# Kernel optimization log

Hardware: AMD Instinct MI355X
Metric: run time of the kernel (lower is better)

## Reference

```python
import jax, jax.numpy as jnp
import numpy as np

N_NODES, F_IN, HID = 50000, 128, 64
N_EDGES = 400000


def _mean_agg(x, ei, n):
    # mean of src features over incoming edges per dst node
    src, dst = ei[0], ei[1]
    s = jax.ops.segment_sum(x[src], dst, num_segments=n)
    cnt = jax.ops.segment_sum(jnp.ones((ei.shape[1],), x.dtype), dst, num_segments=n)
    return s / jnp.maximum(cnt, 1.0)[:, None]


def _conv(x, ei, Wd, Ws, Wu):
    # HeteroGNNConv: mean-aggregate, then lin_dst(x_dst) || lin_src(aggr) -> lin_update
    agg = _mean_agg(x, ei, x.shape[0])
    comb = jnp.concatenate([x @ Wd.T, agg @ Ws.T], axis=-1)  # [N, 2H]
    return comb @ Wu.T


def _bn(x, g, b):
    # BatchNorm1d training-mode, eps=1 (as in the source), biased variance
    m = x.mean(axis=0)
    v = jnp.var(x, axis=0)
    return (x - m) * jax.lax.rsqrt(v + 1.0) * g + b


def setup_inputs() -> dict:
    key = jax.random.key(0)
    ks = jax.random.split(key, 20)
    d = {}
    d['node_feature'] = jax.random.normal(ks[0], (N_NODES, F_IN), dtype=jnp.float32)
    d['edge_index0'] = jax.random.randint(ks[1], (2, N_EDGES), 0, N_NODES, dtype=jnp.int32)
    d['edge_index1'] = jax.random.randint(ks[2], (2, N_EDGES), 0, N_NODES, dtype=jnp.int32)
    i = 3
    for layer, fin in (('l1', F_IN), ('l2', HID)):
        for t in ('t0', 't1'):
            d[f'{layer}{t}_Wd'] = jax.random.normal(ks[i], (HID, fin), dtype=jnp.float32) / np.sqrt(fin); i += 1
            d[f'{layer}{t}_Ws'] = jax.random.normal(ks[i], (HID, fin), dtype=jnp.float32) / np.sqrt(fin); i += 1
            d[f'{layer}{t}_Wu'] = jax.random.normal(ks[i], (HID, 2 * HID), dtype=jnp.float32) / np.sqrt(2 * HID); i += 1
    d['bn1_g'] = jnp.ones((HID,), jnp.float32)
    d['bn1_b'] = jnp.zeros((HID,), jnp.float32)
    d['bn2_g'] = jnp.ones((HID,), jnp.float32)
    d['bn2_b'] = jnp.zeros((HID,), jnp.float32)
    return d


def reference(node_feature, edge_index0, edge_index1,
              l1t0_Wd, l1t0_Ws, l1t0_Wu, l1t1_Wd, l1t1_Ws, l1t1_Wu,
              l2t0_Wd, l2t0_Ws, l2t0_Wu, l2t1_Wd, l2t1_Ws, l2t1_Wu,
              bn1_g, bn1_b, bn2_g, bn2_b):
    x = node_feature
    # layer 1: two message-type convs, mean cross-type aggregation, BN, LeakyReLU
    h = 0.5 * (_conv(x, edge_index0, l1t0_Wd, l1t0_Ws, l1t0_Wu)
               + _conv(x, edge_index1, l1t1_Wd, l1t1_Ws, l1t1_Wu))
    x = jax.nn.leaky_relu(_bn(h, bn1_g, bn1_b), negative_slope=0.01)
    # layer 2
    h = 0.5 * (_conv(x, edge_index0, l2t0_Wd, l2t0_Ws, l2t0_Wu)
               + _conv(x, edge_index1, l2t1_Wd, l2t1_Ws, l2t1_Wu))
    x = jax.nn.leaky_relu(_bn(h, bn2_g, bn2_b), negative_slope=0.01)
    # edge embeddings: [src || dst] per edge, concatenated over edge types
    e0 = jnp.concatenate([x[edge_index0[0]], x[edge_index0[1]]], axis=1)
    e1 = jnp.concatenate([x[edge_index1[0]], x[edge_index1[1]]], axis=1)
    return jnp.concatenate([e0, e1], axis=0)  # [2E, 2H]
```

## Files before the change

kernel.cpp:

```cpp
#include <hip/hip_runtime.h>
#include <math.h>


typedef float f32x4 __attribute__((ext_vector_type(4)));
typedef float f32x2 __attribute__((ext_vector_type(2)));
typedef short bf16x8 __attribute__((ext_vector_type(8)));
typedef unsigned short u16x4 __attribute__((ext_vector_type(4)));

#define NB_SCAN 64

static __device__ __forceinline__ unsigned short f2bf(float f) {
  unsigned int u = __builtin_bit_cast(unsigned int, f);
  unsigned int r = (u + 0x7FFFu + ((u >> 16) & 1u)) >> 16;
  return (unsigned short)r;
}
static __device__ __forceinline__ float bfl(unsigned int u) {
  return __builtin_bit_cast(float, u << 16);
}
static __device__ __forceinline__ float bfh(unsigned int u) {
  return __builtin_bit_cast(float, u & 0xFFFF0000u);
}

__global__ void prep_kernel(const float* __restrict__ Wd10, const float* __restrict__ Ws10,
                            const float* __restrict__ Wu10, const float* __restrict__ Wd11,
                            const float* __restrict__ Ws11, const float* __restrict__ Wu11,
                            unsigned short* __restrict__ Wfb1,
                            const float* __restrict__ Wd20, const float* __restrict__ Ws20,
                            const float* __restrict__ Wu20, const float* __restrict__ Wd21,
                            const float* __restrict__ Ws21, const float* __restrict__ Wu21,
                            unsigned short* __restrict__ Wfb2,
                            int* __restrict__ cnt0, int* __restrict__ cnt1,
                            float* __restrict__ s1, float* __restrict__ s2, int N) {
  int b = blockIdx.x;
  if (b >= 144) {
    int g = (b - 144) * 256 + threadIdx.x;
    if (g < N) { cnt0[g] = 0; cnt1[g] = 0; }
    if (g < 128) { s1[g] = 0.f; s2[g] = 0.f; }
    return;
  }
  const float *Wd0, *Ws0, *Wu0, *Wd1, *Ws1, *Wu1;
  unsigned short* Wfb;
  int K, gid;
  if (b < 96) {
    Wd0 = Wd10; Ws0 = Ws10; Wu0 = Wu10; Wd1 = Wd11; Ws1 = Ws11; Wu1 = Wu11;
    Wfb = Wfb1; K = 128;
    gid = b * 256 + threadIdx.x;
  } else {
    Wd0 = Wd20; Ws0 = Ws20; Wu0 = Wu20; Wd1 = Wd21; Ws1 = Ws21; Wu1 = Wu21;
    Wfb = Wfb2; K = 64;
    gid = (b - 96) * 256 + threadIdx.x;
  }
  if (gid >= 192 * K) return;
  int i = gid / K, j = gid - i * K;
  float s = 0.f;
  if (i < 64) {
#pragma unroll 4
    for (int k = 0; k < 64; ++k)
      s += Wu0[i * 128 + k] * Wd0[k * K + j] + Wu1[i * 128 + k] * Wd1[k * K + j];
  } else if (i < 128) {
    int ii = i - 64;
#pragma unroll 4
    for (int k = 0; k < 64; ++k) s += Wu0[ii * 128 + 64 + k] * Ws0[k * K + j];
  } else {
    int ii = i - 128;
#pragma unroll 4
    for (int k = 0; k < 64; ++k) s += Wu1[ii * 128 + 64 + k] * Ws1[k * K + j];
  }
  Wfb[gid] = f2bf(0.5f * s);
}

__global__ void count_both(const int* __restrict__ dst0, const int* __restrict__ dst1,
                           int* __restrict__ cnt0, int* __restrict__ cnt1, int E, int eg) {
  int b = blockIdx.x;
  bool t1 = b >= eg;
  int e = (t1 ? b - eg : b) * 256 + threadIdx.x;
  if (e >= E) return;
  if (t1) atomicAdd(&cnt1[dst1[e]], 1);
  else atomicAdd(&cnt0[dst0[e]], 1);
}

__global__ __launch_bounds__(256) void scanA(const int* __restrict__ cnt0,
                                             const int* __restrict__ cnt1,
                                             int* __restrict__ bsum, int N, int chunk) {
  int b = blockIdx.x;
  const int* cnt = (b < NB_SCAN) ? cnt0 : cnt1;
  int lb = (b < NB_SCAN) ? b : b - NB_SCAN;
  int lo = lb * chunk, hi = min(lo + chunk, N);
  int s = 0;
  for (int i = lo + threadIdx.x; i < hi; i += 256) s += cnt[i];
  __shared__ int red[256];
  red[threadIdx.x] = s;
  __syncthreads();
  for (int off = 128; off > 0; off >>= 1) {
    if (threadIdx.x < off) red[threadIdx.x] += red[threadIdx.x + off];
    __syncthreads();
  }
  if (threadIdx.x == 0) bsum[b] = red[0];
}

__global__ __launch_bounds__(256) void scanC(const int* __restrict__ cnt0,
                                             const int* __restrict__ cnt1,
                                             const int* __restrict__ bsum,
                                             int* __restrict__ base0, int* __restrict__ base1,
                                             int N, int chunk, int E) {
  int b = blockIdx.x;
  const int* cnt = (b < NB_SCAN) ? cnt0 : cnt1;
  int* base = (b < NB_SCAN) ? base0 : base1;
  int lb = (b < NB_SCAN) ? b : b - NB_SCAN;
  int lo = lb * chunk, hi = min(lo + chunk, N);
  int t = threadIdx.x;
  __shared__ int lsc[2 * NB_SCAN];
  __shared__ int run0s;
  if (t < 2 * NB_SCAN) lsc[t] = bsum[t];
  __syncthreads();
  if (t == 0) {
    int klo = (b < NB_SCAN) ? 0 : NB_SCAN;
    int r = 0;
    for (int k = klo; k < b; ++k) r += lsc[k];
    run0s = r;
  }
  __syncthreads();
  int v[4];
  int ls = 0;
  int i0 = lo + t * 4;
#pragma unroll
  for (int j = 0; j < 4; ++j) {
    v[j] = (i0 + j < hi) ? cnt[i0 + j] : 0;
    ls += v[j];
  }
  __shared__ int l[256];
  l[t] = ls;
  __syncthreads();
  for (int off = 1; off < 256; off <<= 1) {
    int x = l[t];
    if (t >= off) x += l[t - off];
    __syncthreads();
    l[t] = x;
    __syncthreads();
  }
  int run = run0s + l[t] - ls;
#pragma unroll
  for (int j = 0; j < 4; ++j) {
    if (i0 + j < hi) base[i0 + j] = run;
    run += v[j];
  }
  if (t == 0 && lb == NB_SCAN - 1) base[N] = E;
}

__global__ void fill_both(const int* __restrict__ src0, const int* __restrict__ dst0,
                          const int* __restrict__ base0, int* __restrict__ cnt0,
                          int* __restrict__ csr0,
                          const int* __restrict__ src1, const int* __restrict__ dst1,
                          const int* __restrict__ base1, int* __restrict__ cnt1,
                          int* __restrict__ csr1, int E, int eg) {
  int b = blockIdx.x;
  bool t1 = b >= eg;
  int e = (t1 ? b - eg : b) * 256 + threadIdx.x;
  if (e >= E) return;
  const int* src = t1 ? src1 : src0;
  const int* dst = t1 ? dst1 : dst0;
  const int* base = t1 ? base1 : base0;
  int* cnt = t1 ? cnt1 : cnt0;
  int* csr = t1 ? csr1 : csr0;
  int d = dst[e];
  int p = atomicSub(&cnt[d], 1) - 1;
  csr[base[d] + p] = src[e];
}

template <int K, bool BN>
__global__ __launch_bounds__(256) void mm_mfma(const float* __restrict__ xa,
                                               const unsigned short* __restrict__ Wfb,
                                               const float* __restrict__ stats,
                                               const float* __restrict__ gg,
                                               const float* __restrict__ bb, float invN,
                                               float* __restrict__ h,
                                               unsigned short* __restrict__ P0,
                                               unsigned short* __restrict__ P1, int N) {
  constexpr int NKS = K / 32;
  __shared__ float sa[64], sb[64];
  int tid = threadIdx.x;
  if constexpr (BN) {
    if (tid < 64) {
      float m = stats[tid] * invN;
      float v = stats[64 + tid] * invN - m * m;
      float a = gg[tid] * rsqrtf(v + 1.0f);
      sa[tid] = a;
      sb[tid] = bb[tid] - m * a;
    }
    __syncthreads();
  }
  int l = tid & 63;
  int wv = tid >> 6;
  int lr = l & 15;
  int lj = l >> 4;
  int brow = blockIdx.x * 64;
  int wcol = wv * 48;

  bf16x8 B[3 * NKS];
#pragma unroll
  for (int ct = 0; ct < 3; ++ct)
#pragma unroll
    for (int ks = 0; ks < NKS; ++ks) {
      int col = wcol + ct * 16 + lr;
      B[ct * NKS + ks] = *(const bf16x8*)&Wfb[(size_t)col * K + ks * 32 + lj * 8];
    }

  f32x4 acc[4][3];
#pragma unroll
  for (int rt = 0; rt < 4; ++rt)
#pragma unroll
    for (int ct = 0; ct < 3; ++ct) acc[rt][ct] = (f32x4){0.f, 0.f, 0.f, 0.f};

#pragma unroll
  for (int ks = 0; ks < NKS; ++ks) {
    int colbase = ks * 32 + lj * 8;
    bf16x8 A[4];
#pragma unroll
    for (int rt = 0; rt < 4; ++rt) {
      int row = brow + rt * 16 + lr;
      if (row >= N) row = N - 1;
      const float* p = &xa[(size_t)row * K + colbase];
      f32x4 v0 = *(const f32x4*)p;
      f32x4 v1 = *(const f32x4*)(p + 4);
      bf16x8 r;
#pragma unroll
      for (int j = 0; j < 4; ++j) {
        float t0 = v0[j], t1 = v1[j];
        if constexpr (BN) {
          int c0 = colbase + j, c1 = colbase + 4 + j;
          t0 = fmaf(sa[c0], t0, sb[c0]);
          t0 = fmaxf(t0, 0.01f * t0);
          t1 = fmaf(sa[c1], t1, sb[c1]);
          t1 = fmaxf(t1, 0.01f * t1);
        }
        r[j] = (short)f2bf(t0);
        r[4 + j] = (short)f2bf(t1);
      }
      A[rt] = r;
    }
#pragma unroll
    for (int rt = 0; rt < 4; ++rt)
#pragma unroll
      for (int ct = 0; ct < 3; ++ct)
        acc[rt][ct] =
            __builtin_amdgcn_mfma_f32_16x16x32_bf16(A[rt], B[ct * NKS + ks], acc[rt][ct], 0, 0, 0);
  }

#pragma unroll
  for (int rt = 0; rt < 4; ++rt)
#pragma unroll
    for (int ct = 0; ct < 3; ++ct) {
      int gct = (wcol >> 4) + ct;
      int sel = gct >> 2;
      int c0 = (gct & 3) * 16 + lr;
#pragma unroll
      for (int r = 0; r < 4; ++r) {
        int row = brow + rt * 16 + lj * 4 + r;
        if (row < N) {
          if (sel == 0) h[(size_t)row * 64 + c0] = acc[rt][ct][r];
          else if (sel == 1) P0[(size_t)row * 64 + c0] = f2bf(acc[rt][ct][r]);
          else P1[(size_t)row * 64 + c0] = f2bf(acc[rt][ct][r]);
        }
      }
    }
}

__global__ void agg_kernel(float* __restrict__ h, const unsigned short* __restrict__ P0,
                           const unsigned short* __restrict__ P1,
                           const int* __restrict__ csr0, const int* __restrict__ base0,
                           const int* __restrict__ csr1, const int* __restrict__ base1,
                           int N) {
  int gid = blockIdx.x * blockDim.x + threadIdx.x;
  int w = gid >> 5, c = gid & 31;
  if (w >= N) return;
  int co = 2 * c;
  int b0 = base0[w], e0 = base0[w + 1];
  int b1 = base1[w], e1 = base1[w + 1];
  float a0 = 0.f, a1 = 0.f, a2 = 0.f, a3 = 0.f;
  int i = b0;
  for (; i + 4 <= e0; i += 4) {
    int j0 = csr0[i], j1 = csr0[i + 1], j2 = csr0[i + 2], j3 = csr0[i + 3];
    unsigned int u0 = *(const unsigned int*)&P0[(size_t)j0 * 64 + co];
    unsigned int u1 = *(const unsigned int*)&P0[(size_t)j1 * 64 + co];
    unsigned int u2 = *(const unsigned int*)&P0[(size_t)j2 * 64 + co];
    unsigned int u3 = *(const unsigned int*)&P0[(size_t)j3 * 64 + co];
    a0 += bfl(u0); a1 += bfh(u0);
    a2 += bfl(u1); a3 += bfh(u1);
    a0 += bfl(u2); a1 += bfh(u2);
    a2 += bfl(u3); a3 += bfh(u3);
  }
  for (; i < e0; ++i) {
    unsigned int u = *(const unsigned int*)&P0[(size_t)csr0[i] * 64 + co];
    a0 += bfl(u); a1 += bfh(u);
  }
  float i0 = 1.0f / fmaxf((float)(e0 - b0), 1.0f);
  float s0 = (a0 + a2) * i0, s1 = (a1 + a3) * i0;
  a0 = 0.f; a1 = 0.f; a2 = 0.f; a3 = 0.f;
  i = b1;
  for (; i + 4 <= e1; i += 4) {
    int j0 = csr1[i], j1 = csr1[i + 1], j2 = csr1[i + 2], j3 = csr1[i + 3];
    unsigned int u0 = *(const unsigned int*)&P1[(size_t)j0 * 64 + co];
    unsigned int u1 = *(const unsigned int*)&P1[(size_t)j1 * 64 + co];
    unsigned int u2 = *(const unsigned int*)&P1[(size_t)j2 * 64 + co];
    unsigned int u3 = *(const unsigned int*)&P1[(size_t)j3 * 64 + co];
    a0 += bfl(u0); a1 += bfh(u0);
    a2 += bfl(u1); a3 += bfh(u1);
    a0 += bfl(u2); a1 += bfh(u2);
    a2 += bfl(u3); a3 += bfh(u3);
  }
  for (; i < e1; ++i) {
    unsigned int u = *(const unsigned int*)&P1[(size_t)csr1[i] * 64 + co];
    a0 += bfl(u); a1 += bfh(u);
  }
  float i1 = 1.0f / fmaxf((float)(e1 - b1), 1.0f);
  s0 += (a0 + a2) * i1;
  s1 += (a1 + a3) * i1;
  f32x2* hp = (f32x2*)&h[(size_t)w * 64 + co];
  f32x2 hv = *hp;
  hv.x += s0;
  hv.y += s1;
  *hp = hv;
}

__global__ __launch_bounds__(256) void bnstats_kernel(const float* __restrict__ h,
                                                      float* __restrict__ stats, int N) {
  int tid = threadIdx.x;
  int c = tid & 63;
  int part = tid >> 6;
  float s = 0.f, s2 = 0.f;
  for (int r = blockIdx.x * 4 + part; r < N; r += gridDim.x * 4) {
    float v = h[(size_t)r * 64 + c];
    s += v;
    s2 += v * v;
  }
  __shared__ float red[512];
  red[tid] = s;
  red[256 + tid] = s2;
  __syncthreads();
  if (part == 0) {
    s = red[c] + red[64 + c] + red[128 + c] + red[192 + c];
    s2 = red[256 + c] + red[256 + 64 + c] + red[256 + 128 + c] + red[256 + 192 + c];
    atomicAdd(&stats[c], s);
    atomicAdd(&stats[64 + c], s2);
  }
}

__global__ void bnapply_kernel(const float* __restrict__ h, const float* __restrict__ stats,
                               const float* __restrict__ gg, const float* __restrict__ bb,
                               float invN, unsigned short* __restrict__ xo, int N) {
  __shared__ float sa[64], sb[64];
  if (threadIdx.x < 64) {
    int c = threadIdx.x;
    float m = stats[c] * invN;
    float v = stats[64 + c] * invN - m * m;
    float a = gg[c] * rsqrtf(v + 1.0f);
    sa[c] = a;
    sb[c] = bb[c] - m * a;
  }
  __syncthreads();
  int gid = blockIdx.x * blockDim.x + threadIdx.x;
  if (gid >= N * 16) return;
  f32x4 v = ((const f32x4*)h)[gid];
  int c = (gid & 15) * 4;
  u16x4 o;
#pragma unroll
  for (int j = 0; j < 4; ++j) {
    float t = fmaf(sa[c + j], v[j], sb[c + j]);
    o[j] = f2bf(fmaxf(t, 0.01f * t));
  }
  ((u16x4*)xo)[gid] = o;
}

__global__ void gather_kernel(const unsigned short* __restrict__ xc,
                              const int* __restrict__ src0, const int* __restrict__ dst0,
                              const int* __restrict__ src1, const int* __restrict__ dst1,
                              float* __restrict__ out, int E) {
  int gid = blockIdx.x * blockDim.x + threadIdx.x;
  int total = 2 * E * 32;
  if (gid >= total) return;
  int row = gid >> 5, q = gid & 31;
  int e, s, d;
  if (row < E) {
    e = row; s = src0[e]; d = dst0[e];
  } else {
    e = row - E; s = src1[e]; d = dst1[e];
  }
  int node = (q < 16) ? s : d;
  int qq = q & 15;
  u16x4 v = *(const u16x4*)&xc[(size_t)node * 64 + qq * 4];
  f32x4 o;
#pragma unroll
  for (int j = 0; j < 4; ++j) o[j] = bfl((unsigned int)v[j]);
  __builtin_nontemporal_store(o, (f32x4*)out + gid);
}

extern "C" void kernel_launch(void* const* d_in, const int* in_sizes, int n_in,
                              void* d_out, int out_size, void* d_ws, size_t ws_size,
                              hipStream_t stream) {
  const float* x0 = (const float*)d_in[0];
  const int* ei0 = (const int*)d_in[1];
  const int* ei1 = (const int*)d_in[2];
  const float* bn1_g = (const float*)d_in[15];
  const float* bn1_b = (const float*)d_in[16];
  const float* bn2_g = (const float*)d_in[17];
  const float* bn2_b = (const float*)d_in[18];

  const int N = in_sizes[0] / 128;
  const int E = in_sizes[1] / 2;
  const int *src0 = ei0, *dst0 = ei0 + E;
  const int *src1 = ei1, *dst1 = ei1 + E;

  char* wsb = (char*)d_ws;
  size_t off = 0;
  auto alloc = [&](size_t bytes) {
    char* p = wsb + off;
    off = (off + bytes + 255) & ~(size_t)255;
    return (void*)p;
  };
  unsigned short* Wfb1 = (unsigned short*)alloc(192 * 128 * 2);
  unsigned short* Wfb2 = (unsigned short*)alloc(192 * 64 * 2);
  float* stats1 = (float*)alloc(128 * 4);
  float* stats2 = (float*)alloc(128 * 4);
  int* bsum = (int*)alloc(2 * NB_SCAN * 4);
  int* cnt0 = (int*)alloc((size_t)N * 4);
  int* cnt1 = (int*)alloc((size_t)N * 4);
  int* base0 = (int*)alloc(((size_t)N + 1) * 4);
  int* base1 = (int*)alloc(((size_t)N + 1) * 4);
  int* csr0 = (int*)alloc((size_t)E * 4);
  int* csr1 = (int*)alloc((size_t)E * 4);
  float* h = (float*)alloc((size_t)N * 64 * 4);
  float* h2 = (float*)alloc((size_t)N * 64 * 4);
  unsigned short* P0 = (unsigned short*)alloc((size_t)N * 64 * 2);
  unsigned short* P1 = (unsigned short*)alloc((size_t)N * 64 * 2);
  unsigned short* xc2 = (unsigned short*)alloc((size_t)N * 64 * 2);

  const float invN = 1.0f / (float)N;
  const int eg = (E + 255) / 256;
  const int chunk = (N + NB_SCAN - 1) / NB_SCAN;
  const int zb = (N + 255) / 256;

  prep_kernel<<<144 + zb, 256, 0, stream>>>(
      (const float*)d_in[3], (const float*)d_in[4], (const float*)d_in[5],
      (const float*)d_in[6], (const float*)d_in[7], (const float*)d_in[8], Wfb1,
      (const float*)d_in[9], (const float*)d_in[10], (const float*)d_in[11],
      (const float*)d_in[12], (const float*)d_in[13], (const float*)d_in[14], Wfb2,
      cnt0, cnt1, stats1, stats2, N);
  count_both<<<2 * eg, 256, 0, stream>>>(dst0, dst1, cnt0, cnt1, E, eg);
  scanA<<<2 * NB_SCAN, 256, 0, stream>>>(cnt0, cnt1, bsum, N, chunk);
  scanC<<<2 * NB_SCAN, 256, 0, stream>>>(cnt0, cnt1, bsum, base0, base1, N, chunk, E);
  fill_both<<<2 * eg, 256, 0, stream>>>(src0, dst0, base0, cnt0, csr0,
                                        src1, dst1, base1, cnt1, csr1, E, eg);

  const int mmGrid = (N + 63) / 64;
  const int aggGrid = (N * 32 + 255) / 256;

  mm_mfma<128, false><<<mmGrid, 256, 0, stream>>>(x0, Wfb1, nullptr, nullptr, nullptr, 0.f,
                                                  h, P0, P1, N);
  agg_kernel<<<aggGrid, 256, 0, stream>>>(h, P0, P1, csr0, base0, csr1, base1, N);
  bnstats_kernel<<<256, 256, 0, stream>>>(h, stats1, N);

  mm_mfma<64, true><<<mmGrid, 256, 0, stream>>>(h, Wfb2, stats1, bn1_g, bn1_b, invN,
                                                h2, P0, P1, N);
  agg_kernel<<<aggGrid, 256, 0, stream>>>(h2, P0, P1, csr0, base0, csr1, base1, N);
  bnstats_kernel<<<256, 256, 0, stream>>>(h2, stats2, N);
  bnapply_kernel<<<(N * 16 + 255) / 256, 256, 0, stream>>>(h2, stats2, bn2_g, bn2_b, invN,
                                                           xc2, N);

  gather_kernel<<<(2 * E * 32 + 255) / 256, 256, 0, stream>>>(
      xc2, src0, dst0, src1, dst1, (float*)d_out, E);
}
```

Measured before the change: 318.0 us.

## Merge CSR fill into first matmul launch and split agg edge types across half-waves

The CSR fill kernel is folded into the first MFMA matmul launch as extra blocks, so the independent fill work overlaps with the layer-1 projection and one launch goes away. The aggregation kernel now uses 64 lanes per node, with each half-wave handling one edge type, and combines the two partial means with a cross-lane shuffle. This doubles the parallelism of the latency-bound gather and removes the serial second loop. The cost is twice as many threads, and the mixed kernel's register use is set by the larger MFMA body.

```diff
diff --git a/kernel.cpp b/kernel.cpp
--- a/kernel.cpp
+++ b/kernel.cpp
@@ -147,13 +147,15 @@
   if (t == 0 && lb == NB_SCAN - 1) base[N] = E;
 }
 
-__global__ void fill_both(const int* __restrict__ src0, const int* __restrict__ dst0,
-                          const int* __restrict__ base0, int* __restrict__ cnt0,
-                          int* __restrict__ csr0,
-                          const int* __restrict__ src1, const int* __restrict__ dst1,
-                          const int* __restrict__ base1, int* __restrict__ cnt1,
-                          int* __restrict__ csr1, int E, int eg) {
-  int b = blockIdx.x;
+static __device__ __forceinline__ void fill_body(int b, const int* __restrict__ src0,
+                                                 const int* __restrict__ dst0,
+                                                 const int* __restrict__ base0,
+                                                 int* __restrict__ cnt0, int* __restrict__ csr0,
+                                                 const int* __restrict__ src1,
+                                                 const int* __restrict__ dst1,
+                                                 const int* __restrict__ base1,
+                                                 int* __restrict__ cnt1, int* __restrict__ csr1,
+                                                 int E, int eg) {
   bool t1 = b >= eg;
   int e = (t1 ? b - eg : b) * 256 + threadIdx.x;
   if (e >= E) return;
@@ -168,7 +170,7 @@
 }
 
 template <int K, bool BN>
-__global__ __launch_bounds__(256) void mm_mfma(const float* __restrict__ xa,
+static __device__ __forceinline__ void mm_body(int bid, const float* __restrict__ xa,
                                                const unsigned short* __restrict__ Wfb,
                                                const float* __restrict__ stats,
                                                const float* __restrict__ gg,
@@ -193,7 +195,7 @@
   int wv = tid >> 6;
   int lr = l & 15;
   int lj = l >> 4;
-  int brow = blockIdx.x * 64;
+  int brow = bid * 64;
   int wcol = wv * 48;
 
   bf16x8 B[3 * NKS];
@@ -265,61 +267,78 @@
     }
 }
 
+__global__ __launch_bounds__(256) void mm1_fill_kernel(
+    const float* __restrict__ xa, const unsigned short* __restrict__ Wfb,
+    float* __restrict__ h, unsigned short* __restrict__ P0, unsigned short* __restrict__ P1,
+    int N, int mmB,
+    const int* __restrict__ src0, const int* __restrict__ dst0, const int* __restrict__ base0,
+    int* __restrict__ cnt0, int* __restrict__ csr0,
+    const int* __restrict__ src1, const int* __restrict__ dst1, const int* __restrict__ base1,
+    int* __restrict__ cnt1, int* __restrict__ csr1, int E, int eg) {
+  int b = blockIdx.x;
+  if (b < mmB) {
+    mm_body<128, false>(b, xa, Wfb, nullptr, nullptr, nullptr, 0.f, h, P0, P1, N);
+  } else {
+    fill_body(b - mmB, src0, dst0, base0, cnt0, csr0, src1, dst1, base1, cnt1, csr1, E, eg);
+  }
+}
+
+__global__ __launch_bounds__(256) void mm2_kernel(const float* __restrict__ xa,
+                                                  const unsigned short* __restrict__ Wfb,
+                                                  const float* __restrict__ stats,
+                                                  const float* __restrict__ gg,
+                                                  const float* __restrict__ bb, float invN,
+                                                  float* __restrict__ h,
+                                                  unsigned short* __restrict__ P0,
+                                                  unsigned short* __restrict__ P1, int N) {
+  mm_body<64, true>(blockIdx.x, xa, Wfb, stats, gg, bb, invN, h, P0, P1, N);
+}
+
 __global__ void agg_kernel(float* __restrict__ h, const unsigned short* __restrict__ P0,
                            const unsigned short* __restrict__ P1,
                            const int* __restrict__ csr0, const int* __restrict__ base0,
                            const int* __restrict__ csr1, const int* __restrict__ base1,
                            int N) {
   int gid = blockIdx.x * blockDim.x + threadIdx.x;
-  int w = gid >> 5, c = gid & 31;
+  int w = gid >> 6;
   if (w >= N) return;
+  int lane = threadIdx.x & 63;
+  int c = lane & 31;
   int co = 2 * c;
-  int b0 = base0[w], e0 = base0[w + 1];
-  int b1 = base1[w], e1 = base1[w + 1];
+  bool t1 = lane >= 32;
+  const int* csr = t1 ? csr1 : csr0;
+  const int* base = t1 ? base1 : base0;
+  const unsigned short* P = t1 ? P1 : P0;
+  int b0 = base[w], e0 = base[w + 1];
   float a0 = 0.f, a1 = 0.f, a2 = 0.f, a3 = 0.f;
   int i = b0;
   for (; i + 4 <= e0; i += 4) {
-    int j0 = csr0[i], j1 = csr0[i + 1], j2 = csr0[i + 2], j3 = csr0[i + 3];
-    unsigned int u0 = *(const unsigned int*)&P0[(size_t)j0 * 64 + co];
-    unsigned int u1 = *(const unsigned int*)&P0[(size_t)j1 * 64 + co];
-    unsigned int u2 = *(const unsigned int*)&P0[(size_t)j2 * 64 + co];
-    unsigned int u3 = *(const unsigned int*)&P0[(size_t)j3 * 64 + co];
+    int j0 = csr[i], j1 = csr[i + 1], j2 = csr[i + 2], j3 = csr[i + 3];
+    unsigned int u0 = *(const unsigned int*)&P[(size_t)j0 * 64 + co];
+    unsigned int u1 = *(const unsigned int*)&P[(size_t)j1 * 64 + co];
+    unsigned int u2 = *(const unsigned int*)&P[(size_t)j2 * 64 + co];
+    unsigned int u3 = *(const unsigned int*)&P[(size_t)j3 * 64 + co];
     a0 += bfl(u0); a1 += bfh(u0);
     a2 += bfl(u1); a3 += bfh(u1);
     a0 += bfl(u2); a1 += bfh(u2);
     a2 += bfl(u3); a3 += bfh(u3);
   }
   for (; i < e0; ++i) {
-    unsigned int u = *(const unsigned int*)&P0[(size_t)csr0[i] * 64 + co];
+    unsigned int u = *(const unsigned int*)&P[(size_t)csr[i] * 64 + co];
     a0 += bfl(u); a1 += bfh(u);
   }
-  float i0 = 1.0f / fmaxf((float)(e0 - b0), 1.0f);
-  float s0 = (a0 + a2) * i0, s1 = (a1 + a3) * i0;
-  a0 = 0.f; a1 = 0.f; a2 = 0.f; a3 = 0.f;
-  i = b1;
-  for (; i + 4 <= e1; i += 4) {
-    int j0 = csr1[i], j1 = csr1[i + 1], j2 = csr1[i + 2], j3 = csr1[i + 3];
-    unsigned int u0 = *(const unsigned int*)&P1[(size_t)j0 * 64 + co];
-    unsigned int u1 = *(const unsigned int*)&P1[(size_t)j1 * 64 + co];
-    unsigned int u2 = *(const unsigned int*)&P1[(size_t)j2 * 64 + co];
-    unsigned int u3 = *(const unsigned int*)&P1[(size_t)j3 * 64 + co];
-    a0 += bfl(u0); a1 += bfh(u0);
-    a2 += bfl(u1); a3 += bfh(u1);
-    a0 += bfl(u2); a1 += bfh(u2);
-    a2 += bfl(u3); a3 += bfh(u3);
-  }
-  for (; i < e1; ++i) {
-    unsigned int u = *(const unsigned int*)&P1[(size_t)csr1[i] * 64 + co];
-    a0 += bfl(u); a1 += bfh(u);
-  }
-  float i1 = 1.0f / fmaxf((float)(e1 - b1), 1.0f);
-  s0 += (a0 + a2) * i1;
-  s1 += (a1 + a3) * i1;
-  f32x2* hp = (f32x2*)&h[(size_t)w * 64 + co];
-  f32x2 hv = *hp;
-  hv.x += s0;
-  hv.y += s1;
-  *hp = hv;
+  float iv = 1.0f / fmaxf((float)(e0 - b0), 1.0f);
+  float s0 = (a0 + a2) * iv;
+  float s1 = (a1 + a3) * iv;
+  float o0 = __shfl_xor(s0, 32);
+  float o1 = __shfl_xor(s1, 32);
+  if (!t1) {
+    f32x2* hp = (f32x2*)&h[(size_t)w * 64 + co];
+    f32x2 hv = *hp;
+    hv.x += s0 + o0;
+    hv.y += s1 + o1;
+    *hp = hv;
+  }
 }
 
 __global__ __launch_bounds__(256) void bnstats_kernel(const float* __restrict__ h,
@@ -448,19 +467,17 @@
   count_both<<<2 * eg, 256, 0, stream>>>(dst0, dst1, cnt0, cnt1, E, eg);
   scanA<<<2 * NB_SCAN, 256, 0, stream>>>(cnt0, cnt1, bsum, N, chunk);
   scanC<<<2 * NB_SCAN, 256, 0, stream>>>(cnt0, cnt1, bsum, base0, base1, N, chunk, E);
-  fill_both<<<2 * eg, 256, 0, stream>>>(src0, dst0, base0, cnt0, csr0,
-                                        src1, dst1, base1, cnt1, csr1, E, eg);
 
   const int mmGrid = (N + 63) / 64;
-  const int aggGrid = (N * 32 + 255) / 256;
-
-  mm_mfma<128, false><<<mmGrid, 256, 0, stream>>>(x0, Wfb1, nullptr, nullptr, nullptr, 0.f,
-                                                  h, P0, P1, N);
+  const int aggGrid = (N * 64 + 255) / 256;
+
+  mm1_fill_kernel<<<mmGrid + 2 * eg, 256, 0, stream>>>(
+      x0, Wfb1, h, P0, P1, N, mmGrid,
+      src0, dst0, base0, cnt0, csr0, src1, dst1, base1, cnt1, csr1, E, eg);
   agg_kernel<<<aggGrid, 256, 0, stream>>>(h, P0, P1, csr0, base0, csr1, base1, N);
   bnstats_kernel<<<256, 256, 0, stream>>>(h, stats1, N);
 
-  mm_mfma<64, true><<<mmGrid, 256, 0, stream>>>(h, Wfb2, stats1, bn1_g, bn1_b, invN,
-                                                h2, P0, P1, N);
+  mm2_kernel<<<mmGrid, 256, 0, stream>>>(h, Wfb2, stats1, bn1_g, bn1_b, invN, h2, P0, P1, N);
   agg_kernel<<<aggGrid, 256, 0, stream>>>(h2, P0, P1, csr0, base0, csr1, base1, N);
   bnstats_kernel<<<256, 256, 0, stream>>>(h2, stats2, N);
   bnapply_kernel<<<(N * 16 + 255) / 256, 256, 0, stream>>>(h2, stats2, bn2_g, bn2_b, invN,
```

Result: no change. 324.3 us (+2.0%).
